# Kernel tuning notes

Hardware: AMD Instinct MI355X
Metric: run time of the kernel (lower is better)

Reference implementation:

```python
import jax, jax.numpy as jnp
import numpy as np

D_MODEL = 256
D_INNER = 512   # expand_factor * d_model
D_STATE = 64
DT_RANK = 4     # ceil(d_model / 64)
D_CONV = 4
B = 8
L = 144


def setup_inputs() -> dict:
    key = jax.random.key(0)
    ks = jax.random.split(key, 8)
    s = lambda k, shp, sc=0.02: jax.random.normal(k, shp, jnp.float32) * sc
    x = jax.random.normal(ks[0], (B, L, D_MODEL), jnp.float32)
    lastin = jnp.zeros((B, D_INNER, D_STATE), jnp.float32)  # accepted but unused by the scan
    W_in = s(ks[1], (2 * D_INNER, D_MODEL))              # in_proj (no bias)
    conv_w = s(ks[2], (D_INNER, 1, D_CONV), 0.1)          # depthwise conv kernel [O, I/groups, K]
    conv_b = jnp.zeros((D_INNER,), jnp.float32)
    W_x = s(ks[3], (DT_RANK + 2 * D_STATE, D_INNER))      # x_proj (no bias)
    W_dt = s(ks[4], (D_INNER, DT_RANK), 0.1)
    b_dt = jnp.full((D_INNER,), -4.0, jnp.float32)        # softplus -> small dt, like mamba init
    A_log = jnp.log(jnp.tile(jnp.arange(1, D_STATE + 1, dtype=jnp.float32), (D_INNER, 1)))
    Dp = jnp.ones((D_INNER,), jnp.float32)
    W_out = s(ks[5], (D_MODEL, D_INNER))                  # out_proj (no bias)
    return dict(x=x, lastin=lastin, W_in=W_in, conv_w=conv_w, conv_b=conv_b,
                W_x=W_x, W_dt=W_dt, b_dt=b_dt, A_log=A_log, Dp=Dp, W_out=W_out)


def _forward(x, lastin, W_in, conv_w, conv_b, W_x, W_dt, b_dt, A_log, Dp, W_out):
    # in_proj and split
    xz = jnp.einsum('bld,ed->ble', x, W_in)               # [B, L, 2*d_inner]
    ix, z = jnp.split(xz, 2, axis=-1)

    # depthwise causal-ish conv1d: torch padding=2 then slice [:L] == padding (2, 1)
    ix = jnp.swapaxes(ix, 1, 2)                            # [B, d_inner, L]
    ix = jax.lax.conv_general_dilated(
        ix, conv_w, window_strides=(1,), padding=[(2, 1)],
        feature_group_count=D_INNER, dimension_numbers=('NCH', 'OIH', 'NCH'))
    ix = ix + conv_b[None, :, None]
    ix = jnp.swapaxes(ix, 1, 2)                            # [B, L, d_inner]
    ix = jax.nn.silu(ix)

    # ssm parameterization
    A = -jnp.exp(A_log)                                    # [d_inner, d_state]
    dBC = jnp.einsum('bld,ed->ble', ix, W_x)               # [B, L, dt_rank + 2*d_state]
    dt_r = dBC[..., :DT_RANK]
    Bm = dBC[..., DT_RANK:DT_RANK + D_STATE]               # [B, L, d_state]
    Cm = dBC[..., DT_RANK + D_STATE:]                      # [B, L, d_state]
    delta = jax.nn.softplus(jnp.einsum('blr,dr->bld', dt_r, W_dt) + b_dt)  # [B, L, d_inner]

    # discretization
    deltaA = jnp.exp(delta[..., None] * A)                 # [B, L, d_inner, d_state]
    BX = (delta * ix)[..., None] * Bm[:, :, None, :]       # [B, L, d_inner, d_state]

    # sequential selective scan: h_t = deltaA_t * h_{t-1} + BX_t
    def step(h, inp):
        dA_t, bx_t = inp
        h = dA_t * h + bx_t
        return h, h

    h0 = jnp.zeros((x.shape[0], D_INNER, D_STATE), x.dtype)
    _, hs = jax.lax.scan(step, h0, (jnp.moveaxis(deltaA, 1, 0), jnp.moveaxis(BX, 1, 0)))
    # hs: [L, B, d_inner, d_state]

    y = jnp.einsum('lbdn,lbn->bld', hs, jnp.moveaxis(Cm, 1, 0))  # [B, L, d_inner]
    y = y + Dp * ix

    out = jnp.einsum('bld,ed->ble', y * jax.nn.silu(z), W_out)   # [B, L, d_model]
    return out


def reference(x, lastin, W_in, conv_w, conv_b, W_x, W_dt, b_dt, A_log, Dp, W_out):
    return _forward(x, lastin, W_in, conv_w, conv_b, W_x, W_dt, b_dt, A_log, Dp, W_out)
```

## Files before the change

### kernel.cpp

```cpp
#include <hip/hip_runtime.h>

#define B_SZ 8
#define L_SEQ 144
#define NTOK 1152
#define D_MODEL 256
#define D_INNER 512
#define D_STATE 64
#define DT_RANK 4
#define NDBC 132
#define SLAB 152064

#define BM 64
#define BN 64
#define BK 16

typedef __attribute__((ext_vector_type(8))) short bf16x8;
typedef __attribute__((ext_vector_type(4))) float f32x4;

__device__ __forceinline__ void cvt8(const float4& f0, const float4& f1,
                                     int4& hi, int4& lo) {
    const float f[8] = {f0.x, f0.y, f0.z, f0.w, f1.x, f1.y, f1.z, f1.w};
    unsigned h[8], l[8];
#pragma unroll
    for (int e = 0; e < 8; ++e) {
        const unsigned u = __float_as_uint(f[e]);
        const unsigned t = u + 0x7FFFu + ((u >> 16) & 1u);
        h[e] = t >> 16;
        l[e] = __float_as_uint(f[e] - __uint_as_float(t & 0xFFFF0000u)) >> 16;
    }
    hi = make_int4((int)(h[0] | (h[1] << 16)), (int)(h[2] | (h[3] << 16)),
                   (int)(h[4] | (h[5] << 16)), (int)(h[6] | (h[7] << 16)));
    lo = make_int4((int)(l[0] | (l[1] << 16)), (int)(l[2] | (l[3] << 16)),
                   (int)(l[4] | (l[5] << 16)), (int)(l[6] | (l[7] << 16)));
}

#define LW 40
__global__ __launch_bounds__(256) void gemm1_mfma(const float* __restrict__ W_in,
                                                  const float* __restrict__ x,
                                                  float* __restrict__ xz) {
    __shared__ unsigned short Ah[64][LW], Al[64][LW], Bh[64][LW], Bl[64][LW];
    const int tid = threadIdx.x;
    const int m0 = blockIdx.y * 64, n0 = blockIdx.x * 64;
    const int r = tid >> 2, kq = (tid & 3) * 8;
    const int w = tid >> 6, lane = tid & 63;
    const int wm = (w & 1) * 32, wn = (w >> 1) * 32;
    const int fr = lane & 15, fk = (lane >> 4) * 8;
    f32x4 acc[2][2] = {};
    float4 a0, a1, b0, b1;

    auto loadG = [&](const int k0) {
        const float* ap = W_in + (size_t)(m0 + r) * D_MODEL + k0 + kq;
        const float* bp = x    + (size_t)(n0 + r) * D_MODEL + k0 + kq;
        a0 = *(const float4*)ap; a1 = *(const float4*)(ap + 4);
        b0 = *(const float4*)bp; b1 = *(const float4*)(bp + 4);
    };

    loadG(0);
    for (int k0 = 0; k0 < D_MODEL; k0 += 32) {
        int4 hi, lo;
        __syncthreads();
        cvt8(a0, a1, hi, lo);
        *(int4*)&Ah[r][kq] = hi; *(int4*)&Al[r][kq] = lo;
        cvt8(b0, b1, hi, lo);
        *(int4*)&Bh[r][kq] = hi; *(int4*)&Bl[r][kq] = lo;
        __syncthreads();
        if (k0 + 32 < D_MODEL) loadG(k0 + 32);
        bf16x8 ah[2], al[2], bh[2], bl[2];
#pragma unroll
        for (int i = 0; i < 2; ++i) {
            ah[i] = *(const bf16x8*)&Ah[wm + 16 * i + fr][fk];
            al[i] = *(const bf16x8*)&Al[wm + 16 * i + fr][fk];
            bh[i] = *(const bf16x8*)&Bh[wn + 16 * i + fr][fk];
            bl[i] = *(const bf16x8*)&Bl[wn + 16 * i + fr][fk];
        }
#pragma unroll
        for (int i = 0; i < 2; ++i)
#pragma unroll
            for (int j = 0; j < 2; ++j) {
                acc[i][j] = __builtin_amdgcn_mfma_f32_16x16x32_bf16(ah[i], bh[j], acc[i][j], 0, 0, 0);
                acc[i][j] = __builtin_amdgcn_mfma_f32_16x16x32_bf16(ah[i], bl[j], acc[i][j], 0, 0, 0);
                acc[i][j] = __builtin_amdgcn_mfma_f32_16x16x32_bf16(al[i], bh[j], acc[i][j], 0, 0, 0);
            }
    }
    const int orow = (lane >> 4) * 4;
#pragma unroll
    for (int i = 0; i < 2; ++i)
#pragma unroll
        for (int j = 0; j < 2; ++j)
#pragma unroll
            for (int q = 0; q < 4; ++q)
                xz[(size_t)(m0 + wm + 16 * i + orow + q) * NTOK
                   + n0 + wn + 16 * j + fr] = acc[i][j][q];
}

__global__ __launch_bounds__(256) void gemm3_mfma(const unsigned short* __restrict__ ghi,
                                                  const unsigned short* __restrict__ glo,
                                                  const float* __restrict__ W_out,
                                                  float* __restrict__ slab) {
    const int tid = threadIdx.x;
    const int n0 = blockIdx.x * 64, m0 = blockIdx.y * 64;
    const int kbeg = blockIdx.z * 64;
    const int w = tid >> 6, lane = tid & 63;
    const int wm = (w & 1) * 32, wn = (w >> 1) * 32;
    const int fr = lane & 15, fk = (lane >> 4) * 8;
    f32x4 acc[2][2] = {};
    slab += (size_t)blockIdx.z * (NTOK * D_MODEL);
#pragma unroll
    for (int ks = 0; ks < 2; ++ks) {
        const int k0 = kbeg + ks * 32;
        bf16x8 ah[2], al[2], bh[2], bl[2];
#pragma unroll
        for (int i = 0; i < 2; ++i) {
            const size_t ao = (size_t)(m0 + wm + 16 * i + fr) * D_INNER + k0 + fk;
            ah[i] = *(const bf16x8*)(ghi + ao);
            al[i] = *(const bf16x8*)(glo + ao);
        }
#pragma unroll
        for (int j = 0; j < 2; ++j) {
            const float* bp = W_out + (size_t)(n0 + wn + 16 * j + fr) * D_INNER + k0 + fk;
            int4 hi, lo;
            cvt8(*(const float4*)bp, *(const float4*)(bp + 4), hi, lo);
            bh[j] = *(bf16x8*)&hi;
            bl[j] = *(bf16x8*)&lo;
        }
#pragma unroll
        for (int i = 0; i < 2; ++i)
#pragma unroll
            for (int j = 0; j < 2; ++j) {
                acc[i][j] = __builtin_amdgcn_mfma_f32_16x16x32_bf16(ah[i], bh[j], acc[i][j], 0, 0, 0);
                acc[i][j] = __builtin_amdgcn_mfma_f32_16x16x32_bf16(ah[i], bl[j], acc[i][j], 0, 0, 0);
                acc[i][j] = __builtin_amdgcn_mfma_f32_16x16x32_bf16(al[i], bh[j], acc[i][j], 0, 0, 0);
            }
    }
    const int orow = (lane >> 4) * 4;
#pragma unroll
    for (int i = 0; i < 2; ++i)
#pragma unroll
        for (int j = 0; j < 2; ++j)
#pragma unroll
            for (int q = 0; q < 4; ++q)
                slab[(size_t)(m0 + wm + 16 * i + orow + q) * D_MODEL
                     + n0 + wn + 16 * j + fr] = acc[i][j][q];
}

__device__ __forceinline__ int bc_perm(const int p) {
    return (p < DT_RANK) ? p
         : (((p - DT_RANK) & 1) ? (DT_RANK + D_STATE + ((p - DT_RANK) >> 1))
                                : (DT_RANK + ((p - DT_RANK) >> 1)));
}

template<bool A_MK, bool GN, bool CONV, bool PERM>
__global__ __launch_bounds__(256) void gemm_k(const float* __restrict__ A,
                                              const float* __restrict__ Bm,
                                              float* __restrict__ C,
                                              const int N, const int lda, const int ldb,
                                              const int ldc,
                                              const float* __restrict__ cw,
                                              const float* __restrict__ cb,
                                              const int kslab, const size_t sstride) {
    __shared__ float As[BK][BM + 4];
    __shared__ float Bs[BK][BN + 4];
    const int tid = threadIdx.x;
    const int m0 = blockIdx.y * BM;
    const int n0 = blockIdx.x * BN;
    const int kbeg = blockIdx.z * kslab;
    const int kend = kbeg + kslab;
    const int ty = tid >> 4, tx = tid & 15;
    const int lrow = tid >> 2, kq = (tid & 3) * 4;
    const int kk = tid >> 4, cc = (tid & 15) * 4;
    const int brow = PERM ? bc_perm(n0 + lrow) : (n0 + lrow);
    float acc[4][4] = {};
    float4 av, bv, cw4;
    float xm2 = 0.f, xm1 = 0.f, xp4 = 0.f, cbv = 0.f;

    auto loadA = [&](const int k0) {
        if (A_MK) {
            av = *(const float4*)(A + (size_t)(m0 + lrow) * lda + k0 + kq);
        } else {
            const float* row = A + (size_t)(k0 + kk) * lda + m0 + cc;
            av = *(const float4*)row;
            if (CONV) {
                const int t = (m0 + cc) % L_SEQ;
                xm2 = (t > 0) ? row[-2] : 0.f;
                xm1 = (t > 0) ? row[-1] : 0.f;
                xp4 = (t < L_SEQ - 4) ? row[4] : 0.f;
                cw4 = *(const float4*)(cw + (k0 + kk) * 4);
                cbv = cb[k0 + kk];
            }
        }
        if (!GN || (n0 + lrow) < N)
            bv = *(const float4*)(Bm + (size_t)brow * ldb + k0 + kq);
    };

    auto storeLDS = [&]() {
        if (A_MK) {
            As[kq + 0][lrow] = av.x; As[kq + 1][lrow] = av.y;
            As[kq + 2][lrow] = av.z; As[kq + 3][lrow] = av.w;
        } else if (CONV) {
            const float in7[7] = {xm2, xm1, av.x, av.y, av.z, av.w, xp4};
            float4 o;
            float* op = &o.x;
#pragma unroll
            for (int j = 0; j < 4; ++j) {
                float s = cbv;
                s = fmaf(cw4.x, in7[j + 0], s);
                s = fmaf(cw4.y, in7[j + 1], s);
                s = fmaf(cw4.z, in7[j + 2], s);
                s = fmaf(cw4.w, in7[j + 3], s);
                op[j] = s * __builtin_amdgcn_rcpf(1.f + __expf(-s));
            }
            *(float4*)&As[kk][cc] = o;
        } else {
            *(float4*)&As[kk][cc] = av;
        }
        Bs[kq + 0][lrow] = bv.x; Bs[kq + 1][lrow] = bv.y;
        Bs[kq + 2][lrow] = bv.z; Bs[kq + 3][lrow] = bv.w;
    };

    bv = make_float4(0.f, 0.f, 0.f, 0.f);
    loadA(kbeg);
    for (int k0 = kbeg; k0 < kend; k0 += BK) {
        __syncthreads();
        storeLDS();
        __syncthreads();
        if (k0 + BK < kend) loadA(k0 + BK);
#pragma unroll
        for (int k = 0; k < BK; ++k) {
            const float4 a4 = *(const float4*)&As[k][ty * 4];
            const float4 b4 = *(const float4*)&Bs[k][tx * 4];
            const float a_[4] = {a4.x, a4.y, a4.z, a4.w};
            const float b_[4] = {b4.x, b4.y, b4.z, b4.w};
#pragma unroll
            for (int i = 0; i < 4; ++i)
#pragma unroll
                for (int j = 0; j < 4; ++j)
                    acc[i][j] = fmaf(a_[i], b_[j], acc[i][j]);
        }
    }
    C += (size_t)blockIdx.z * sstride;
#pragma unroll
    for (int i = 0; i < 4; ++i) {
        const int gm = m0 + ty * 4 + i;
        const int gn = n0 + tx * 4;
        if (!GN || gn < N)
            *(float4*)(C + (size_t)gm * ldc + gn) =
                make_float4(acc[i][0], acc[i][1], acc[i][2], acc[i][3]);
    }
}

__global__ __launch_bounds__(256) void reduce8_k(const float4* __restrict__ in,
                                                 float4* __restrict__ out,
                                                 const int n4, const int s4) {
    const int i = blockIdx.x * 256 + threadIdx.x;
    if (i >= n4) return;
    float4 a = in[i];
#pragma unroll
    for (int s = 1; s < 8; ++s) {
        const float4 b = in[i + s * s4];
        a.x += b.x; a.y += b.y; a.z += b.z; a.w += b.w;
    }
    out[i] = a;
}

__device__ __forceinline__ float bcast(const float v, const int i) {
    return __int_as_float(__builtin_amdgcn_readlane(__float_as_int(v), i));
}

template<int CNT>
__device__ __forceinline__ void scan_chunk(const float* __restrict__ dBC,
                                           const float* __restrict__ xz,
                                           unsigned short* __restrict__ ghi,
                                           unsigned short* __restrict__ glo,
                                           float (*__restrict__ Pw)[65],
                                           const int d, const int base, const int t0,
                                           const float An2, const float4 wdt,
                                           const float bdt, const float dpv,
                                           const float4 cw4, const float cbv,
                                           const int lane, float& h) {
    float delta_r = 0.f, dix_r = 0.f, dpix_r = 0.f, sz_r = 0.f;
    if (lane < CNT) {
        const int t = t0 + lane;
        const int tok = base + t;
        const float* row = xz + (size_t)d * NTOK + tok;
        float s0 = cbv;
        if (t >= 2) s0 = fmaf(cw4.x, row[-2], s0);
        if (t >= 1) s0 = fmaf(cw4.y, row[-1], s0);
        s0 = fmaf(cw4.z, row[0], s0);
        if (t < L_SEQ - 1) s0 = fmaf(cw4.w, row[1], s0);
        const float ixv = s0 * __builtin_amdgcn_rcpf(1.f + __expf(-s0));

        const float4 dt4 = *(const float4*)(dBC + (size_t)tok * NDBC);
        float s = fmaf(dt4.x, wdt.x, bdt);
        s = fmaf(dt4.y, wdt.y, s);
        s = fmaf(dt4.z, wdt.z, s);
        s = fmaf(dt4.w, wdt.w, s);
        const float delta = fmaxf(s, 0.f) + __logf(1.f + __expf(-fabsf(s)));
        const float zv = xz[(size_t)(D_INNER + d) * NTOK + tok];
        delta_r = delta;
        dix_r   = delta * ixv;
        dpix_r  = dpv * ixv;
        sz_r    = zv * __builtin_amdgcn_rcpf(1.f + __expf(-zv));
    }
#pragma unroll
    for (int i = 0; i < CNT; ++i) {
        const float2 bc = *(const float2*)(dBC + (size_t)(base + t0 + i) * NDBC
                                           + DT_RANK + 2 * lane);
        const float dlt = bcast(delta_r, i);
        const float dxv = bcast(dix_r, i);
        const float dA = __builtin_amdgcn_exp2f(dlt * An2);
        h = fmaf(dA, h, dxv * bc.x);
        Pw[i][lane] = h * bc.y;
    }
    const int tl = lane & 31, hf = lane >> 5;
    float s2 = 0.f;
    if (tl < CNT) {
#pragma unroll
        for (int j = 0; j < 32; ++j) s2 += Pw[tl][hf * 32 + j];
    }
    s2 += __shfl_xor(s2, 32, 64);
    if (hf == 0 && tl < CNT) {
        const float g = (s2 + dpix_r) * sz_r;
        const unsigned u = __float_as_uint(g);
        const unsigned t = u + 0x7FFFu + ((u >> 16) & 1u);
        const size_t o = (size_t)(base + t0 + tl) * D_INNER + d;
        ghi[o] = (unsigned short)(t >> 16);
        glo[o] = (unsigned short)(__float_as_uint(
                     g - __uint_as_float(t & 0xFFFF0000u)) >> 16);
    }
}

__global__ __launch_bounds__(256) void scan_k(const float* __restrict__ dBC,
                                              const float* __restrict__ xz,
                                              const float* __restrict__ W_dt,
                                              const float* __restrict__ b_dt,
                                              const float* __restrict__ A_log,
                                              const float* __restrict__ Dp,
                                              const float* __restrict__ conv_w,
                                              const float* __restrict__ conv_b,
                                              unsigned short* __restrict__ ghi,
                                              unsigned short* __restrict__ glo) {
    __shared__ float P[4][32][65];
    const int w = threadIdx.x >> 6, lane = threadIdx.x & 63;
    const int b = blockIdx.x >> 7, dg = blockIdx.x & 127;
    const int d = (dg << 2) | w;
    const int base = b * L_SEQ;
    const float An2 = -__expf(A_log[(d << 6) + lane]) * 1.44269504088896f;
    const float4 wdt = *(const float4*)(W_dt + (d << 2));
    const float bdt = b_dt[d], dpv = Dp[d];
    const float4 cw4 = *(const float4*)(conv_w + (d << 2));
    const float cbv = conv_b[d];
    float h = 0.f;
    scan_chunk<32>(dBC, xz, ghi, glo, P[w], d, base, 0,   An2, wdt, bdt, dpv, cw4, cbv, lane, h);
    scan_chunk<32>(dBC, xz, ghi, glo, P[w], d, base, 32,  An2, wdt, bdt, dpv, cw4, cbv, lane, h);
    scan_chunk<32>(dBC, xz, ghi, glo, P[w], d, base, 64,  An2, wdt, bdt, dpv, cw4, cbv, lane, h);
    scan_chunk<32>(dBC, xz, ghi, glo, P[w], d, base, 96,  An2, wdt, bdt, dpv, cw4, cbv, lane, h);
    scan_chunk<16>(dBC, xz, ghi, glo, P[w], d, base, 128, An2, wdt, bdt, dpv, cw4, cbv, lane, h);
}

extern "C" void kernel_launch(void* const* d_in, const int* in_sizes, int n_in,
                              void* d_out, int out_size, void* d_ws, size_t ws_size,
                              hipStream_t stream) {
    const float* x      = (const float*)d_in[0];
    const float* W_in   = (const float*)d_in[2];
    const float* conv_w = (const float*)d_in[3];
    const float* conv_b = (const float*)d_in[4];
    const float* W_x    = (const float*)d_in[5];
    const float* W_dt   = (const float*)d_in[6];
    const float* b_dt   = (const float*)d_in[7];
    const float* A_log  = (const float*)d_in[8];
    const float* Dp     = (const float*)d_in[9];
    const float* W_out  = (const float*)d_in[10];
    float* out = (float*)d_out;

    float* ws  = (float*)d_ws;
    float* xz  = ws;
    float* dBC = xz + 1179648;
    float* sl3 = dBC + 152064;
    unsigned short* ghi = (unsigned short*)(sl3 + 8 * SLAB);
    unsigned short* glo = ghi + NTOK * D_INNER;
    float* sl6 = (float*)(glo + NTOK * D_INNER);

    gemm1_mfma<<<dim3(18, 16), 256, 0, stream>>>(W_in, x, xz);
    gemm_k<false, true, true, true><<<dim3(3, 18, 8), 256, 0, stream>>>(
        xz, W_x, sl3, NDBC, NTOK, D_INNER, NDBC, conv_w, conv_b, 64, (size_t)SLAB);
    reduce8_k<<<dim3(149), 256, 0, stream>>>((const float4*)sl3, (float4*)dBC,
                                             NTOK * NDBC / 4, NTOK * NDBC / 4);
    scan_k<<<dim3(B_SZ * 128), 256, 0, stream>>>(dBC, xz, W_dt, b_dt, A_log, Dp,
                                                 conv_w, conv_b, ghi, glo);
    gemm3_mfma<<<dim3(4, 18, 8), 256, 0, stream>>>(ghi, glo, W_out, sl6);
    reduce8_k<<<dim3(288), 256, 0, stream>>>((const float4*)sl6, (float4*)out,
                                             NTOK * D_MODEL / 4, NTOK * D_MODEL / 4);
}
```

Before: 136.4 us.

## Move conv+x_proj GEMM to split-bf16 MFMA and pack gated output hi/lo

Replaces the scalar FP32 tiled gemm_k for the conv+SiLU+x_proj stage with an MFMA kernel. It applies the depthwise conv and SiLU while staging, splits A and B into bf16 hi/lo pairs in LDS and uses three bf16 MFMAs per tile to keep near-FP32 accuracy. Separately, the scan's gated output is now written as one packed 32-bit word per element, the hi/lo bf16 halves that were two separate short arrays. gemm3 unpacks these words, so each element is a single store and a single load instead of two scattered ones. The hi/lo split approximates FP32 (the lo*lo term is dropped), and the conv boundary logic is widened to 8-element rows.

```diff
diff --git a/kernel.cpp b/kernel.cpp
--- a/kernel.cpp
+++ b/kernel.cpp
@@ -10,10 +10,6 @@
 #define NDBC 132
 #define SLAB 152064
 
-#define BM 64
-#define BN 64
-#define BK 16
-
 typedef __attribute__((ext_vector_type(8))) short bf16x8;
 typedef __attribute__((ext_vector_type(4))) float f32x4;
 
@@ -32,6 +28,21 @@
                    (int)(h[4] | (h[5] << 16)), (int)(h[6] | (h[7] << 16)));
     lo = make_int4((int)(l[0] | (l[1] << 16)), (int)(l[2] | (l[3] << 16)),
                    (int)(l[4] | (l[5] << 16)), (int)(l[6] | (l[7] << 16)));
+}
+
+__device__ __forceinline__ void unpack8(const int4& p0, const int4& p1,
+                                        bf16x8& hv, bf16x8& lv) {
+    const unsigned u[8] = {(unsigned)p0.x, (unsigned)p0.y, (unsigned)p0.z,
+                           (unsigned)p0.w, (unsigned)p1.x, (unsigned)p1.y,
+                           (unsigned)p1.z, (unsigned)p1.w};
+    int h[4], l[4];
+#pragma unroll
+    for (int i = 0; i < 4; ++i) {
+        h[i] = (int)((u[2 * i] >> 16) | (u[2 * i + 1] & 0xFFFF0000u));
+        l[i] = (int)((u[2 * i] & 0xFFFFu) | (u[2 * i + 1] << 16));
+    }
+    hv = *(bf16x8*)h;
+    lv = *(bf16x8*)l;
 }
 
 #define LW 40
@@ -93,8 +104,104 @@
                    + n0 + wn + 16 * j + fr] = acc[i][j][q];
 }
 
-__global__ __launch_bounds__(256) void gemm3_mfma(const unsigned short* __restrict__ ghi,
-                                                  const unsigned short* __restrict__ glo,
+__device__ __forceinline__ int bc_perm(const int p) {
+    return (p < DT_RANK) ? p
+         : (((p - DT_RANK) & 1) ? (DT_RANK + D_STATE + ((p - DT_RANK) >> 1))
+                                : (DT_RANK + ((p - DT_RANK) >> 1)));
+}
+
+__global__ __launch_bounds__(256) void gemm2_mfma(const float* __restrict__ xz,
+                                                  const float* __restrict__ W_x,
+                                                  float* __restrict__ slab,
+                                                  const float* __restrict__ cw,
+                                                  const float* __restrict__ cb) {
+    __shared__ unsigned short Ah[64][LW], Al[64][LW], Bh[64][LW], Bl[64][LW];
+    const int tid = threadIdx.x;
+    const int n0 = blockIdx.x * 64;
+    const int m0 = blockIdx.y * 64;
+    const int kbeg = blockIdx.z * 64;
+    const int ar = tid >> 3, ac8 = (tid & 7) * 8;
+    const int br = tid >> 2, bq8 = (tid & 3) * 8;
+    const int brow = bc_perm(n0 + br);
+    const int w = tid >> 6, lane = tid & 63;
+    const int wm = (w & 1) * 32, wn = (w >> 1) * 32;
+    const int fr = lane & 15, fk = (lane >> 4) * 8;
+    const int t = (m0 + ac8) % L_SEQ;
+    f32x4 acc[2][2] = {};
+    slab += (size_t)blockIdx.z * SLAB;
+
+#pragma unroll
+    for (int ks = 0; ks < 2; ++ks) {
+        const int k0 = kbeg + ks * 32;
+        const int d = k0 + ar;
+        const float* row = xz + (size_t)d * NTOK + m0 + ac8;
+        const float4 a0 = *(const float4*)row;
+        const float4 a1 = *(const float4*)(row + 4);
+        const float xm2 = (t > 0) ? row[-2] : 0.f;
+        const float xm1 = (t > 0) ? row[-1] : 0.f;
+        const float xp8 = (t < L_SEQ - 8) ? row[8] : 0.f;
+        const float4 cw4 = *(const float4*)(cw + d * 4);
+        const float cbv = cb[d];
+        float4 bv0 = make_float4(0.f, 0.f, 0.f, 0.f), bv1 = bv0;
+        if (n0 + br < NDBC) {
+            const float* bp = W_x + (size_t)brow * D_INNER + k0 + bq8;
+            bv0 = *(const float4*)bp; bv1 = *(const float4*)(bp + 4);
+        }
+        __syncthreads();
+        {
+            const float in[11] = {xm2, xm1, a0.x, a0.y, a0.z, a0.w,
+                                  a1.x, a1.y, a1.z, a1.w, xp8};
+#pragma unroll
+            for (int j = 0; j < 8; ++j) {
+                float s = cbv;
+                s = fmaf(cw4.x, in[j + 0], s);
+                s = fmaf(cw4.y, in[j + 1], s);
+                s = fmaf(cw4.z, in[j + 2], s);
+                s = fmaf(cw4.w, in[j + 3], s);
+                const float g = s * __builtin_amdgcn_rcpf(1.f + __expf(-s));
+                const unsigned u = __float_as_uint(g);
+                const unsigned tt = u + 0x7FFFu + ((u >> 16) & 1u);
+                Ah[ac8 + j][ar] = (unsigned short)(tt >> 16);
+                Al[ac8 + j][ar] = (unsigned short)(__float_as_uint(
+                                     g - __uint_as_float(tt & 0xFFFF0000u)) >> 16);
+            }
+            int4 hi, lo;
+            cvt8(bv0, bv1, hi, lo);
+            *(int4*)&Bh[br][bq8] = hi; *(int4*)&Bl[br][bq8] = lo;
+        }
+        __syncthreads();
+        bf16x8 ah[2], al[2], bh[2], bl[2];
+#pragma unroll
+        for (int i = 0; i < 2; ++i) {
+            ah[i] = *(const bf16x8*)&Ah[wm + 16 * i + fr][fk];
+            al[i] = *(const bf16x8*)&Al[wm + 16 * i + fr][fk];
+            bh[i] = *(const bf16x8*)&Bh[wn + 16 * i + fr][fk];
+            bl[i] = *(const bf16x8*)&Bl[wn + 16 * i + fr][fk];
+        }
+#pragma unroll
+        for (int i = 0; i < 2; ++i)
+#pragma unroll
+            for (int j = 0; j < 2; ++j) {
+                acc[i][j] = __builtin_amdgcn_mfma_f32_16x16x32_bf16(ah[i], bh[j], acc[i][j], 0, 0, 0);
+                acc[i][j] = __builtin_amdgcn_mfma_f32_16x16x32_bf16(ah[i], bl[j], acc[i][j], 0, 0, 0);
+                acc[i][j] = __builtin_amdgcn_mfma_f32_16x16x32_bf16(al[i], bh[j], acc[i][j], 0, 0, 0);
+            }
+    }
+    const int orow = (lane >> 4) * 4;
+#pragma unroll
+    for (int i = 0; i < 2; ++i)
+#pragma unroll
+        for (int j = 0; j < 2; ++j) {
+            const int gn = n0 + wn + 16 * j + fr;
+            if (gn < NDBC)
+#pragma unroll
+                for (int q = 0; q < 4; ++q)
+                    slab[(size_t)(m0 + wm + 16 * i + orow + q) * NDBC + gn]
+                        = acc[i][j][q];
+        }
+}
+
+__global__ __launch_bounds__(256) void gemm3_mfma(const unsigned* __restrict__ gpk,
                                                   const float* __restrict__ W_out,
                                                   float* __restrict__ slab) {
     const int tid = threadIdx.x;
@@ -111,9 +218,8 @@
         bf16x8 ah[2], al[2], bh[2], bl[2];
 #pragma unroll
         for (int i = 0; i < 2; ++i) {
-            const size_t ao = (size_t)(m0 + wm + 16 * i + fr) * D_INNER + k0 + fk;
-            ah[i] = *(const bf16x8*)(ghi + ao);
-            al[i] = *(const bf16x8*)(glo + ao);
+            const unsigned* ap = gpk + (size_t)(m0 + wm + 16 * i + fr) * D_INNER + k0 + fk;
+            unpack8(*(const int4*)ap, *(const int4*)(ap + 4), ah[i], al[i]);
         }
 #pragma unroll
         for (int j = 0; j < 2; ++j) {
@@ -143,111 +249,6 @@
                      + n0 + wn + 16 * j + fr] = acc[i][j][q];
 }
 
-__device__ __forceinline__ int bc_perm(const int p) {
-    return (p < DT_RANK) ? p
-         : (((p - DT_RANK) & 1) ? (DT_RANK + D_STATE + ((p - DT_RANK) >> 1))
-                                : (DT_RANK + ((p - DT_RANK) >> 1)));
-}
-
-template<bool A_MK, bool GN, bool CONV, bool PERM>
-__global__ __launch_bounds__(256) void gemm_k(const float* __restrict__ A,
-                                              const float* __restrict__ Bm,
-                                              float* __restrict__ C,
-                                              const int N, const int lda, const int ldb,
-                                              const int ldc,
-                                              const float* __restrict__ cw,
-                                              const float* __restrict__ cb,
-                                              const int kslab, const size_t sstride) {
-    __shared__ float As[BK][BM + 4];
-    __shared__ float Bs[BK][BN + 4];
-    const int tid = threadIdx.x;
-    const int m0 = blockIdx.y * BM;
-    const int n0 = blockIdx.x * BN;
-    const int kbeg = blockIdx.z * kslab;
-    const int kend = kbeg + kslab;
-    const int ty = tid >> 4, tx = tid & 15;
-    const int lrow = tid >> 2, kq = (tid & 3) * 4;
-    const int kk = tid >> 4, cc = (tid & 15) * 4;
-    const int brow = PERM ? bc_perm(n0 + lrow) : (n0 + lrow);
-    float acc[4][4] = {};
-    float4 av, bv, cw4;
-    float xm2 = 0.f, xm1 = 0.f, xp4 = 0.f, cbv = 0.f;
-
-    auto loadA = [&](const int k0) {
-        if (A_MK) {
-            av = *(const float4*)(A + (size_t)(m0 + lrow) * lda + k0 + kq);
-        } else {
-            const float* row = A + (size_t)(k0 + kk) * lda + m0 + cc;
-            av = *(const float4*)row;
-            if (CONV) {
-                const int t = (m0 + cc) % L_SEQ;
-                xm2 = (t > 0) ? row[-2] : 0.f;
-                xm1 = (t > 0) ? row[-1] : 0.f;
-                xp4 = (t < L_SEQ - 4) ? row[4] : 0.f;
-                cw4 = *(const float4*)(cw + (k0 + kk) * 4);
-                cbv = cb[k0 + kk];
-            }
-        }
-        if (!GN || (n0 + lrow) < N)
-            bv = *(const float4*)(Bm + (size_t)brow * ldb + k0 + kq);
-    };
-
-    auto storeLDS = [&]() {
-        if (A_MK) {
-            As[kq + 0][lrow] = av.x; As[kq + 1][lrow] = av.y;
-            As[kq + 2][lrow] = av.z; As[kq + 3][lrow] = av.w;
-        } else if (CONV) {
-            const float in7[7] = {xm2, xm1, av.x, av.y, av.z, av.w, xp4};
-            float4 o;
-            float* op = &o.x;
-#pragma unroll
-            for (int j = 0; j < 4; ++j) {
-                float s = cbv;
-                s = fmaf(cw4.x, in7[j + 0], s);
-                s = fmaf(cw4.y, in7[j + 1], s);
-                s = fmaf(cw4.z, in7[j + 2], s);
-                s = fmaf(cw4.w, in7[j + 3], s);
-                op[j] = s * __builtin_amdgcn_rcpf(1.f + __expf(-s));
-            }
-            *(float4*)&As[kk][cc] = o;
-        } else {
-            *(float4*)&As[kk][cc] = av;
-        }
-        Bs[kq + 0][lrow] = bv.x; Bs[kq + 1][lrow] = bv.y;
-        Bs[kq + 2][lrow] = bv.z; Bs[kq + 3][lrow] = bv.w;
-    };
-
-    bv = make_float4(0.f, 0.f, 0.f, 0.f);
-    loadA(kbeg);
-    for (int k0 = kbeg; k0 < kend; k0 += BK) {
-        __syncthreads();
-        storeLDS();
-        __syncthreads();
-        if (k0 + BK < kend) loadA(k0 + BK);
-#pragma unroll
-        for (int k = 0; k < BK; ++k) {
-            const float4 a4 = *(const float4*)&As[k][ty * 4];
-            const float4 b4 = *(const float4*)&Bs[k][tx * 4];
-            const float a_[4] = {a4.x, a4.y, a4.z, a4.w};
-            const float b_[4] = {b4.x, b4.y, b4.z, b4.w};
-#pragma unroll
-            for (int i = 0; i < 4; ++i)
-#pragma unroll
-                for (int j = 0; j < 4; ++j)
-                    acc[i][j] = fmaf(a_[i], b_[j], acc[i][j]);
-        }
-    }
-    C += (size_t)blockIdx.z * sstride;
-#pragma unroll
-    for (int i = 0; i < 4; ++i) {
-        const int gm = m0 + ty * 4 + i;
-        const int gn = n0 + tx * 4;
-        if (!GN || gn < N)
-            *(float4*)(C + (size_t)gm * ldc + gn) =
-                make_float4(acc[i][0], acc[i][1], acc[i][2], acc[i][3]);
-    }
-}
-
 __global__ __launch_bounds__(256) void reduce8_k(const float4* __restrict__ in,
                                                  float4* __restrict__ out,
                                                  const int n4, const int s4) {
@@ -269,8 +270,7 @@
 template<int CNT>
 __device__ __forceinline__ void scan_chunk(const float* __restrict__ dBC,
                                            const float* __restrict__ xz,
-                                           unsigned short* __restrict__ ghi,
-                                           unsigned short* __restrict__ glo,
+                                           unsigned* __restrict__ gpk,
                                            float (*__restrict__ Pw)[65],
                                            const int d, const int base, const int t0,
                                            const float An2, const float4 wdt,
@@ -322,10 +322,9 @@
         const float g = (s2 + dpix_r) * sz_r;
         const unsigned u = __float_as_uint(g);
         const unsigned t = u + 0x7FFFu + ((u >> 16) & 1u);
-        const size_t o = (size_t)(base + t0 + tl) * D_INNER + d;
-        ghi[o] = (unsigned short)(t >> 16);
-        glo[o] = (unsigned short)(__float_as_uint(
-                     g - __uint_as_float(t & 0xFFFF0000u)) >> 16);
+        const unsigned lo16 = __float_as_uint(
+            g - __uint_as_float(t & 0xFFFF0000u)) >> 16;
+        gpk[(size_t)(base + t0 + tl) * D_INNER + d] = (t & 0xFFFF0000u) | lo16;
     }
 }
 
@@ -337,8 +336,7 @@
                                               const float* __restrict__ Dp,
                                               const float* __restrict__ conv_w,
                                               const float* __restrict__ conv_b,
-                                              unsigned short* __restrict__ ghi,
-                                              unsigned short* __restrict__ glo) {
+                                              unsigned* __restrict__ gpk) {
     __shared__ float P[4][32][65];
     const int w = threadIdx.x >> 6, lane = threadIdx.x & 63;
     const int b = blockIdx.x >> 7, dg = blockIdx.x & 127;
@@ -350,11 +348,11 @@
     const float4 cw4 = *(const float4*)(conv_w + (d << 2));
     const float cbv = conv_b[d];
     float h = 0.f;
-    scan_chunk<32>(dBC, xz, ghi, glo, P[w], d, base, 0,   An2, wdt, bdt, dpv, cw4, cbv, lane, h);
-    scan_chunk<32>(dBC, xz, ghi, glo, P[w], d, base, 32,  An2, wdt, bdt, dpv, cw4, cbv, lane, h);
-    scan_chunk<32>(dBC, xz, ghi, glo, P[w], d, base, 64,  An2, wdt, bdt, dpv, cw4, cbv, lane, h);
-    scan_chunk<32>(dBC, xz, ghi, glo, P[w], d, base, 96,  An2, wdt, bdt, dpv, cw4, cbv, lane, h);
-    scan_chunk<16>(dBC, xz, ghi, glo, P[w], d, base, 128, An2, wdt, bdt, dpv, cw4, cbv, lane, h);
+    scan_chunk<32>(dBC, xz, gpk, P[w], d, base, 0,   An2, wdt, bdt, dpv, cw4, cbv, lane, h);
+    scan_chunk<32>(dBC, xz, gpk, P[w], d, base, 32,  An2, wdt, bdt, dpv, cw4, cbv, lane, h);
+    scan_chunk<32>(dBC, xz, gpk, P[w], d, base, 64,  An2, wdt, bdt, dpv, cw4, cbv, lane, h);
+    scan_chunk<32>(dBC, xz, gpk, P[w], d, base, 96,  An2, wdt, bdt, dpv, cw4, cbv, lane, h);
+    scan_chunk<16>(dBC, xz, gpk, P[w], d, base, 128, An2, wdt, bdt, dpv, cw4, cbv, lane, h);
 }
 
 extern "C" void kernel_launch(void* const* d_in, const int* in_sizes, int n_in,
@@ -376,18 +374,16 @@
     float* xz  = ws;
     float* dBC = xz + 1179648;
     float* sl3 = dBC + 152064;
-    unsigned short* ghi = (unsigned short*)(sl3 + 8 * SLAB);
-    unsigned short* glo = ghi + NTOK * D_INNER;
-    float* sl6 = (float*)(glo + NTOK * D_INNER);
+    unsigned* gpk = (unsigned*)(sl3 + 8 * SLAB);
+    float* sl6 = (float*)(gpk + NTOK * D_INNER);
 
     gemm1_mfma<<<dim3(18, 16), 256, 0, stream>>>(W_in, x, xz);
-    gemm_k<false, true, true, true><<<dim3(3, 18, 8), 256, 0, stream>>>(
-        xz, W_x, sl3, NDBC, NTOK, D_INNER, NDBC, conv_w, conv_b, 64, (size_t)SLAB);
+    gemm2_mfma<<<dim3(3, 18, 8), 256, 0, stream>>>(xz, W_x, sl3, conv_w, conv_b);
     reduce8_k<<<dim3(149), 256, 0, stream>>>((const float4*)sl3, (float4*)dBC,
                                              NTOK * NDBC / 4, NTOK * NDBC / 4);
     scan_k<<<dim3(B_SZ * 128), 256, 0, stream>>>(dBC, xz, W_dt, b_dt, A_log, Dp,
-                                                 conv_w, conv_b, ghi, glo);
-    gemm3_mfma<<<dim3(4, 18, 8), 256, 0, stream>>>(ghi, glo, W_out, sl6);
+                                                 conv_w, conv_b, gpk);
+    gemm3_mfma<<<dim3(4, 18, 8), 256, 0, stream>>>(gpk, W_out, sl6);
     reduce8_k<<<dim3(288), 256, 0, stream>>>((const float4*)sl6, (float4*)out,
                                              NTOK * D_MODEL / 4, NTOK * D_MODEL / 4);
 }
```

Measured after the change: 130.5 us. 4.4% less time.
